# Kernel tuning notes

Measured on AMD Instinct MI355X. Metric: run time of the kernel, lower is better.

Reference implementation:

```python
import jax, jax.numpy as jnp
import numpy as np

B, N, G, E = 4, 8192, 512, 512
D = 3 * E  # fused channel dim = 1536
BN_EPS = 1e-5


def setup_inputs() -> dict:
    key = jax.random.key(0)
    ks = jax.random.split(key, 8)
    f32 = jnp.float32
    return {
        "xyz": jax.random.normal(ks[0], (B, N, 3), f32),
        "centers": jax.random.normal(ks[1], (B, G, 3), f32),
        "H4": jax.random.normal(ks[2], (B, G, E), f32),
        "H8": jax.random.normal(ks[3], (B, G, E), f32),
        "H12": jax.random.normal(ks[4], (B, G, E), f32),
        "w1": jax.random.normal(ks[5], (512, D), f32) * 0.02,
        "b1": jnp.zeros((512,), f32),
        "g1": jnp.ones((512,), f32),
        "be1": jnp.zeros((512,), f32),
        "m1": jnp.zeros((512,), f32),
        "v1": jnp.ones((512,), f32),
        "w2": jax.random.normal(ks[6], (512, 512), f32) * 0.02,
        "b2": jnp.zeros((512,), f32),
        "g2": jnp.ones((512,), f32),
        "be2": jnp.zeros((512,), f32),
        "m2": jnp.zeros((512,), f32),
        "v2": jnp.ones((512,), f32),
    }


def _bn(x, gamma, beta, mean, var):
    # BatchNorm1d, eval mode with running stats (per-channel, last axis)
    return (x - mean) * jax.lax.rsqrt(var + BN_EPS) * gamma + beta


def reference(xyz, centers, H4, H8, H12,
              w1, b1, g1, be1, m1, v1,
              w2, b2, g2, be2, m2, v2):
    fused = jnp.concatenate([H4, H8, H12], axis=-1)  # [B,G,D]
    # squared pairwise distances [B,N,G]
    d = (jnp.sum(xyz * xyz, axis=-1, keepdims=True)
         + jnp.sum(centers * centers, axis=-1)[:, None, :]
         - 2.0 * jnp.einsum('bnc,bgc->bng', xyz, centers))
    neg_d3, idx = jax.lax.top_k(-d, 3)  # 3 smallest distances, ascending
    d3 = -neg_d3  # [B,N,3]
    recip = 1.0 / (d3 + 1e-8)
    w = recip / jnp.sum(recip, axis=-1, keepdims=True)  # [B,N,3]
    # gather neighbor features: [B,N,3,D]
    gathered = jax.vmap(lambda f, i: f[i])(fused, idx)
    interp = jnp.einsum('bnk,bnkd->bnd', w, gathered)  # [B,N,D]
    # 1x1 conv == per-point linear; conv -> BN(eval) -> ReLU, twice
    h = jax.nn.relu(_bn(interp @ w1.T + b1, g1, be1, m1, v1))
    h = jax.nn.relu(_bn(h @ w2.T + b2, g2, be2, m2, v2))
    return h  # [B,N,512]
```

## Files before the change

kernel.cpp:

```cpp
#include <hip/hip_runtime.h>
#include <stdint.h>

#define NP 8192
#define NG 512
#define DF 1536

using f32x4    = __attribute__((ext_vector_type(4))) float;
using bf16x8   = __attribute__((ext_vector_type(8))) __bf16;
using ushort8v = __attribute__((ext_vector_type(8))) unsigned short;


__device__ __forceinline__ unsigned short f32_to_bf16(float f) {
  unsigned int u = __float_as_uint(f);
  u += 0x7fffu + ((u >> 16) & 1u);
  return (unsigned short)(u >> 16);
}
__device__ __forceinline__ float bf2f(unsigned short u) {
  return __uint_as_float(((unsigned)u) << 16);
}

struct FusedArgs {
  const float *xyz, *centers, *H4, *H8, *H12, *w1, *w2;
  const float *g1, *be1, *m1, *v1, *g2, *be2, *m2, *v2, *b1, *b2;
  unsigned short *fswz, *w1s, *w2s, *Amatb;
  int *nidx; float *nw, *s1, *t1, *s2, *t2;
  float *outp;
};

__device__ void phase_knn(const FusedArgs& a, char* smem, int w) {
  const int tid = threadIdx.x;
  float4* cs = (float4*)smem;
  const int b = w >> 7;
  for (int i = tid; i < NG; i += 256) {
    float c0 = a.centers[((size_t)b * NG + i) * 3 + 0];
    float c1 = a.centers[((size_t)b * NG + i) * 3 + 1];
    float c2 = a.centers[((size_t)b * NG + i) * 3 + 2];
    float4 v; v.x = c0; v.y = c1; v.z = c2; v.w = c0 * c0 + c1 * c1 + c2 * c2;
    cs[(i >> 7) * 129 + (i & 127)] = v;
  }
  __syncthreads();
  const int t = (w & 127) * 256 + tid;
  const int p = t >> 2, q = t & 3;
  const size_t pi = (size_t)b * NP + p;
  const float x0 = a.xyz[pi * 3 + 0], x1 = a.xyz[pi * 3 + 1], x2 = a.xyz[pi * 3 + 2];
  const float xx = x0 * x0 + x1 * x1 + x2 * x2;
  float d0 = 3.4e38f, d1 = 3.4e38f, d2 = 3.4e38f;
  int i0 = 0, i1 = 0, i2 = 0;
  const int gbase = q * 128;
  const float4* csq = cs + q * 129;
#pragma unroll 4
  for (int j = 0; j < 128; ++j) {
    float4 c = csq[j];
    float d = xx + c.w - 2.0f * (x0 * c.x + x1 * c.y + x2 * c.z);
    int g = gbase + j;
    bool c0 = d < d0, c1 = d < d1, c2 = d < d2;
    float nd2 = c1 ? d1 : (c2 ? d : d2); int ni2 = c1 ? i1 : (c2 ? g : i2);
    float nd1 = c0 ? d0 : (c1 ? d : d1); int ni1 = c0 ? i0 : (c1 ? g : i1);
    d0 = c0 ? d : d0;                    i0 = c0 ? g : i0;
    d1 = nd1; i1 = ni1; d2 = nd2; i2 = ni2;
  }
#pragma unroll
  for (int off = 1; off <= 2; off <<= 1) {
    float e0 = __shfl_xor(d0, off), e1 = __shfl_xor(d1, off), e2 = __shfl_xor(d2, off);
    int j0 = __shfl_xor(i0, off), j1 = __shfl_xor(i1, off), j2 = __shfl_xor(i2, off);
#pragma unroll
    for (int s = 0; s < 3; ++s) {
      float e = (s == 0) ? e0 : (s == 1 ? e1 : e2);
      int   j = (s == 0) ? j0 : (s == 1 ? j1 : j2);
      bool c0 = (e < d0) || (e == d0 && j < i0);
      bool c1 = (e < d1) || (e == d1 && j < i1);
      bool c2 = (e < d2) || (e == d2 && j < i2);
      float nd2 = c1 ? d1 : (c2 ? e : d2); int ni2 = c1 ? i1 : (c2 ? j : i2);
      float nd1 = c0 ? d0 : (c1 ? e : d1); int ni1 = c0 ? i0 : (c1 ? j : i1);
      d0 = c0 ? e : d0;                    i0 = c0 ? j : i0;
      d1 = nd1; i1 = ni1; d2 = nd2; i2 = ni2;
    }
  }
  if (q == 0) {
    float r0 = 1.0f / (d0 + 1e-8f), r1 = 1.0f / (d1 + 1e-8f), r2 = 1.0f / (d2 + 1e-8f);
    float inv = 1.0f / (r0 + r1 + r2);
    a.nw[pi * 3 + 0] = r0 * inv; a.nw[pi * 3 + 1] = r1 * inv; a.nw[pi * 3 + 2] = r2 * inv;
    a.nidx[pi * 3 + 0] = i0; a.nidx[pi * 3 + 1] = i1; a.nidx[pi * 3 + 2] = i2;
  }
}

__device__ void phase_casts(const FusedArgs& a, int u) {
  const int tid = threadIdx.x;
  if (u < 2048) {
    const int qd = (u - 512) * 256 + tid;
    const int L = qd & 63, t2 = qd >> 6;
    const int kc = t2 % 48, mg = t2 / 48;
    const int m = mg * 16 + (L & 15);
    const int k = kc * 32 + (L >> 4) * 8;
    const float* src = (k < 512) ? a.H4 : (k < 1024 ? a.H8 : a.H12);
    const float* sp = &src[(size_t)m * 512 + (k & 511)];
    float4 va = *(const float4*)sp, vb = *(const float4*)(sp + 4);
    ushort8v o;
    o[0] = f32_to_bf16(va.x); o[1] = f32_to_bf16(va.y);
    o[2] = f32_to_bf16(va.z); o[3] = f32_to_bf16(va.w);
    o[4] = f32_to_bf16(vb.x); o[5] = f32_to_bf16(vb.y);
    o[6] = f32_to_bf16(vb.z); o[7] = f32_to_bf16(vb.w);
    *(ushort8v*)&a.fswz[((size_t)(mg * 48 + kc)) * 512 + L * 8] = o;
  } else if (u < 2432) {
    const int qd = (u - 2048) * 256 + tid;
    const int L = qd & 63, t2 = qd >> 6;
    const int kc = t2 % 48, ng = t2 / 48;
    const int n = ng * 16 + (L & 15);
    const int k = kc * 32 + (L >> 4) * 8;
    const float* sp = &a.w1[(size_t)n * 1536 + k];
    float4 va = *(const float4*)sp, vb = *(const float4*)(sp + 4);
    ushort8v o;
    o[0] = f32_to_bf16(va.x); o[1] = f32_to_bf16(va.y);
    o[2] = f32_to_bf16(va.z); o[3] = f32_to_bf16(va.w);
    o[4] = f32_to_bf16(vb.x); o[5] = f32_to_bf16(vb.y);
    o[6] = f32_to_bf16(vb.z); o[7] = f32_to_bf16(vb.w);
    *(ushort8v*)&a.w1s[((size_t)(ng * 48 + kc)) * 512 + L * 8] = o;
  } else if (u < 2560) {
    const int qd = (u - 2432) * 256 + tid;
    const int L = qd & 63, t2 = qd >> 6;
    const int kc = t2 & 15, ng = t2 >> 4;
    const int n = ng * 16 + (L & 15);
    const int k = kc * 32 + (L >> 4) * 8;
    const float* sp = &a.w2[(size_t)n * 512 + k];
    float4 va = *(const float4*)sp, vb = *(const float4*)(sp + 4);
    ushort8v o;
    o[0] = f32_to_bf16(va.x); o[1] = f32_to_bf16(va.y);
    o[2] = f32_to_bf16(va.z); o[3] = f32_to_bf16(va.w);
    o[4] = f32_to_bf16(vb.x); o[5] = f32_to_bf16(vb.y);
    o[6] = f32_to_bf16(vb.z); o[7] = f32_to_bf16(vb.w);
    *(ushort8v*)&a.w2s[((size_t)(ng * 16 + kc)) * 512 + L * 8] = o;
  } else {
    for (int i = tid; i < 512; i += 256) {
      float sa = a.g1[i] / sqrtf(a.v1[i] + 1e-5f);
      a.s1[i] = sa; a.t1[i] = a.be1[i] - a.m1[i] * sa;
      float sb = a.g2[i] / sqrtf(a.v2[i] + 1e-5f);
      a.s2[i] = sb; a.t2[i] = a.be2[i] - a.m2[i] * sb;
    }
  }
}

__device__ void phase_gemm1(const FusedArgs& a, char* smem, int blk) {
  float* red = (float*)smem;
  const int tid = threadIdx.x, lane = tid & 63, wv = tid >> 6;
  const int m0 = (blk >> 3) * 32;
  const int n0 = (blk & 7) * 64;
  const unsigned short* Ap = a.fswz + ((size_t)(m0 >> 4) * 48 + wv * 12) * 512 + lane * 8;
  const unsigned short* Bp = a.w1s  + ((size_t)(n0 >> 4) * 48 + wv * 12) * 512 + lane * 8;

  f32x4 acc[2][4];
#pragma unroll
  for (int i = 0; i < 2; ++i)
#pragma unroll
    for (int j = 0; j < 4; ++j) acc[i][j] = (f32x4){0.f, 0.f, 0.f, 0.f};

  bf16x8 af[2], bfr[4], afn[2], bfn[4];
#pragma unroll
  for (int i = 0; i < 2; ++i)
    af[i]  = __builtin_bit_cast(bf16x8, *(const ushort8v*)(Ap + (size_t)i * 48 * 512));
#pragma unroll
  for (int i = 0; i < 4; ++i)
    bfr[i] = __builtin_bit_cast(bf16x8, *(const ushort8v*)(Bp + (size_t)i * 48 * 512));
#pragma unroll 1
  for (int kc = 0; kc < 12; ++kc) {
    if (kc < 11) {
#pragma unroll
      for (int i = 0; i < 2; ++i)
        afn[i] = __builtin_bit_cast(bf16x8, *(const ushort8v*)(Ap + (size_t)i * 48 * 512 + (kc + 1) * 512));
#pragma unroll
      for (int i = 0; i < 4; ++i)
        bfn[i] = __builtin_bit_cast(bf16x8, *(const ushort8v*)(Bp + (size_t)i * 48 * 512 + (kc + 1) * 512));
    }
#pragma unroll
    for (int mi = 0; mi < 2; ++mi)
#pragma unroll
      for (int ni = 0; ni < 4; ++ni)
        acc[mi][ni] = __builtin_amdgcn_mfma_f32_16x16x32_bf16(af[mi], bfr[ni], acc[mi][ni], 0, 0, 0);
#pragma unroll
    for (int i = 0; i < 2; ++i) af[i] = afn[i];
#pragma unroll
    for (int i = 0; i < 4; ++i) bfr[i] = bfn[i];
  }

  for (int w = 0; w < 4; ++w) {
    if (wv == w) {
#pragma unroll
      for (int mi = 0; mi < 2; ++mi)
#pragma unroll
        for (int ni = 0; ni < 4; ++ni) {
          int col = ni * 16 + (lane & 15);
#pragma unroll
          for (int r = 0; r < 4; ++r) {
            int row = mi * 16 + (lane >> 4) * 4 + r;
            if (w == 0) red[row * 65 + col] = acc[mi][ni][r];
            else        red[row * 65 + col] += acc[mi][ni][r];
          }
        }
    }
    __syncthreads();
  }
  const int row = tid >> 3;
  const int col = (tid & 7) * 8;
  ushort8v o;
#pragma unroll
  for (int j = 0; j < 8; ++j) {
    int n = n0 + col + j;
    float v = red[row * 65 + col + j];
    o[j] = f32_to_bf16(a.s1[n] * (v + a.b1[n]) + a.t1[n]);
  }
  *(ushort8v*)&a.Amatb[(size_t)(m0 + row) * 512 + n0 + col] = o;
}

__global__ __launch_bounds__(1024, 4) void k_mega(FusedArgs a) {
  __shared__ __align__(16) unsigned short hl[128 * 512];
  const int tid = threadIdx.x, lane = tid & 63, wv = tid >> 6;
  const int xcd = blockIdx.x & 7, slot = blockIdx.x >> 3;
  const int m0 = (xcd * 32 + slot) * 128;

  {
    const int rg = wv >> 1, kc0 = (wv & 1) * 8;
    const int p = m0 + rg * 16 + (lane & 15);
    const int b = p >> 13;
    const int i0 = a.nidx[p * 3 + 0], i1 = a.nidx[p * 3 + 1], i2 = a.nidx[p * 3 + 2];
    const float w0 = a.nw[p * 3 + 0], w1v = a.nw[p * 3 + 1], w2v = a.nw[p * 3 + 2];
    const int co = kc0 * 32 + (lane >> 4) * 8;
    const unsigned short* A0 = a.Amatb + ((size_t)(b * 512 + i0)) * 512 + co;
    const unsigned short* A1 = a.Amatb + ((size_t)(b * 512 + i1)) * 512 + co;
    const unsigned short* A2 = a.Amatb + ((size_t)(b * 512 + i2)) * 512 + co;
    unsigned short* wp = hl + (size_t)(rg * 16 + kc0) * 512 + lane * 8;
#pragma unroll 4
    for (int j = 0; j < 8; ++j) {
      ushort8v u0 = *(const ushort8v*)(A0 + j * 32);
      ushort8v u1 = *(const ushort8v*)(A1 + j * 32);
      ushort8v u2 = *(const ushort8v*)(A2 + j * 32);
      ushort8v o;
#pragma unroll
      for (int jj = 0; jj < 8; ++jj) {
        float v = w0 * bf2f(u0[jj]) + w1v * bf2f(u1[jj]) + w2v * bf2f(u2[jj]);
        o[jj] = f32_to_bf16(fmaxf(v, 0.f));
      }
      *(ushort8v*)(wp + (size_t)j * 512) = o;
    }
  }
  __syncthreads();

  const int n0 = wv * 32;
  const unsigned short* Bbase = a.w2s + (size_t)(n0 >> 4) * 16 * 512 + lane * 8;

  f32x4 acc[8][2];
#pragma unroll
  for (int i = 0; i < 8; ++i) {
    acc[i][0] = (f32x4){0.f, 0.f, 0.f, 0.f};
    acc[i][1] = (f32x4){0.f, 0.f, 0.f, 0.f};
  }

  bf16x8 bfr[2], bfn[2];
  bfr[0] = __builtin_bit_cast(bf16x8, *(const ushort8v*)(Bbase));
  bfr[1] = __builtin_bit_cast(bf16x8, *(const ushort8v*)(Bbase + (size_t)16 * 512));
#pragma unroll 1
  for (int kc = 0; kc < 16; ++kc) {
    if (kc < 15) {
      bfn[0] = __builtin_bit_cast(bf16x8,
          *(const ushort8v*)(Bbase + (size_t)(kc + 1) * 512));
      bfn[1] = __builtin_bit_cast(bf16x8,
          *(const ushort8v*)(Bbase + (size_t)(16 + kc + 1) * 512));
    }
#pragma unroll
    for (int mi = 0; mi < 8; ++mi) {
      bf16x8 af = __builtin_bit_cast(bf16x8,
          *(const ushort8v*)(hl + (size_t)(mi * 16 + kc) * 512 + lane * 8));
      acc[mi][0] = __builtin_amdgcn_mfma_f32_16x16x32_bf16(af, bfr[0], acc[mi][0], 0, 0, 0);
      acc[mi][1] = __builtin_amdgcn_mfma_f32_16x16x32_bf16(af, bfr[1], acc[mi][1], 0, 0, 0);
    }
    bfr[0] = bfn[0]; bfr[1] = bfn[1];
  }

#pragma unroll
  for (int mi = 0; mi < 8; ++mi) {
    int mbase = m0 + mi * 16 + (lane >> 4) * 4;
#pragma unroll
    for (int ni = 0; ni < 2; ++ni) {
      int n = n0 + ni * 16 + (lane & 15);
      float s = a.s2[n], bb = a.b2[n], t = a.t2[n];
      f32x4 v = acc[mi][ni];
#pragma unroll
      for (int r = 0; r < 4; ++r)
        __builtin_nontemporal_store(fmaxf(s * (v[r] + bb) + t, 0.f),
                                    &a.outp[(size_t)(mbase + r) * 512 + n]);
    }
  }
}

__global__ __launch_bounds__(256) void k_casts(FusedArgs a) {
  phase_casts(a, 512 + blockIdx.x);
}
__global__ __launch_bounds__(256) void k_g1knn(FusedArgs a) {
  __shared__ __align__(16) char smem[8448];
  if (blockIdx.x < 512) phase_gemm1(a, smem, blockIdx.x);
  else                  phase_knn(a, smem, blockIdx.x - 512);
}

extern "C" void kernel_launch(void* const* d_in, const int* in_sizes, int n_in,
                              void* d_out, int out_size, void* d_ws, size_t ws_size,
                              hipStream_t stream) {
  char* ws = (char*)d_ws;
  FusedArgs a;
  a.xyz     = (const float*)d_in[0];
  a.centers = (const float*)d_in[1];
  a.H4      = (const float*)d_in[2];
  a.H8      = (const float*)d_in[3];
  a.H12     = (const float*)d_in[4];
  a.w1      = (const float*)d_in[5];
  a.b1      = (const float*)d_in[6];
  a.g1      = (const float*)d_in[7];
  a.be1     = (const float*)d_in[8];
  a.m1      = (const float*)d_in[9];
  a.v1      = (const float*)d_in[10];
  a.w2      = (const float*)d_in[11];
  a.b2      = (const float*)d_in[12];
  a.g2      = (const float*)d_in[13];
  a.be2     = (const float*)d_in[14];
  a.m2      = (const float*)d_in[15];
  a.v2      = (const float*)d_in[16];
  a.fswz  = (unsigned short*)(ws);
  a.w1s   = (unsigned short*)(ws + 6291456);
  a.w2s   = (unsigned short*)(ws + 7864320);
  a.Amatb = (unsigned short*)(ws + 8388608);
  a.nidx  = (int*)           (ws + 10485760);
  a.nw    = (float*)         (ws + 10878976);
  a.s1    = (float*)         (ws + 11272192);
  a.t1 = a.s1 + 512; a.s2 = a.t1 + 512; a.t2 = a.s2 + 512;
  a.outp  = (float*)d_out;

  k_casts<<<2049, 256, 0, stream>>>(a);
  k_g1knn<<<1024, 256, 0, stream>>>(a);
  k_mega <<< 256, 1024, 0, stream>>>(a);
}
```

Baseline: 162.0 us.

## Pipeline neighbor gather into LDS with MFMA over K quarters

Splits the gather-interpolate-ReLU stage of the mega kernel into four K-quarters and interleaves them with the second GEMM. Each quarter's global loads are issued before the MFMA work on the previous quarter, so gather latency overlaps with matrix math instead of running as one serial phase. This adds three extra block-wide barriers and keeps more registers live for the in-flight loads, which may pressure occupancy at 1024 threads.

Result: slower. 179.0 us (+10.5%).

```diff
diff --git a/kernel.cpp b/kernel.cpp
--- a/kernel.cpp
+++ b/kernel.cpp
@@ -216,32 +216,16 @@
   const int xcd = blockIdx.x & 7, slot = blockIdx.x >> 3;
   const int m0 = (xcd * 32 + slot) * 128;
 
-  {
-    const int rg = wv >> 1, kc0 = (wv & 1) * 8;
-    const int p = m0 + rg * 16 + (lane & 15);
-    const int b = p >> 13;
-    const int i0 = a.nidx[p * 3 + 0], i1 = a.nidx[p * 3 + 1], i2 = a.nidx[p * 3 + 2];
-    const float w0 = a.nw[p * 3 + 0], w1v = a.nw[p * 3 + 1], w2v = a.nw[p * 3 + 2];
-    const int co = kc0 * 32 + (lane >> 4) * 8;
-    const unsigned short* A0 = a.Amatb + ((size_t)(b * 512 + i0)) * 512 + co;
-    const unsigned short* A1 = a.Amatb + ((size_t)(b * 512 + i1)) * 512 + co;
-    const unsigned short* A2 = a.Amatb + ((size_t)(b * 512 + i2)) * 512 + co;
-    unsigned short* wp = hl + (size_t)(rg * 16 + kc0) * 512 + lane * 8;
-#pragma unroll 4
-    for (int j = 0; j < 8; ++j) {
-      ushort8v u0 = *(const ushort8v*)(A0 + j * 32);
-      ushort8v u1 = *(const ushort8v*)(A1 + j * 32);
-      ushort8v u2 = *(const ushort8v*)(A2 + j * 32);
-      ushort8v o;
-#pragma unroll
-      for (int jj = 0; jj < 8; ++jj) {
-        float v = w0 * bf2f(u0[jj]) + w1v * bf2f(u1[jj]) + w2v * bf2f(u2[jj]);
-        o[jj] = f32_to_bf16(fmaxf(v, 0.f));
-      }
-      *(ushort8v*)(wp + (size_t)j * 512) = o;
-    }
-  }
-  __syncthreads();
+  const int rg = wv >> 1;
+  const int p = m0 + rg * 16 + (lane & 15);
+  const int b = p >> 13;
+  const int i0 = a.nidx[p * 3 + 0], i1 = a.nidx[p * 3 + 1], i2 = a.nidx[p * 3 + 2];
+  const float w0 = a.nw[p * 3 + 0], w1v = a.nw[p * 3 + 1], w2v = a.nw[p * 3 + 2];
+  const int cg8 = (lane >> 4) * 8;
+  const unsigned short* A0 = a.Amatb + ((size_t)(b * 512 + i0)) * 512 + cg8;
+  const unsigned short* A1 = a.Amatb + ((size_t)(b * 512 + i1)) * 512 + cg8;
+  const unsigned short* A2 = a.Amatb + ((size_t)(b * 512 + i2)) * 512 + cg8;
+  const int kcw = (wv & 1) * 2;
 
   const int n0 = wv * 32;
   const unsigned short* Bbase = a.w2s + (size_t)(n0 >> 4) * 16 * 512 + lane * 8;
@@ -253,26 +237,78 @@
     acc[i][1] = (f32x4){0.f, 0.f, 0.f, 0.f};
   }
 
-  bf16x8 bfr[2], bfn[2];
-  bfr[0] = __builtin_bit_cast(bf16x8, *(const ushort8v*)(Bbase));
-  bfr[1] = __builtin_bit_cast(bf16x8, *(const ushort8v*)(Bbase + (size_t)16 * 512));
-#pragma unroll 1
-  for (int kc = 0; kc < 16; ++kc) {
-    if (kc < 15) {
-      bfn[0] = __builtin_bit_cast(bf16x8,
-          *(const ushort8v*)(Bbase + (size_t)(kc + 1) * 512));
-      bfn[1] = __builtin_bit_cast(bf16x8,
-          *(const ushort8v*)(Bbase + (size_t)(16 + kc + 1) * 512));
-    }
-#pragma unroll
-    for (int mi = 0; mi < 8; ++mi) {
-      bf16x8 af = __builtin_bit_cast(bf16x8,
-          *(const ushort8v*)(hl + (size_t)(mi * 16 + kc) * 512 + lane * 8));
-      acc[mi][0] = __builtin_amdgcn_mfma_f32_16x16x32_bf16(af, bfr[0], acc[mi][0], 0, 0, 0);
-      acc[mi][1] = __builtin_amdgcn_mfma_f32_16x16x32_bf16(af, bfr[1], acc[mi][1], 0, 0, 0);
-    }
-    bfr[0] = bfn[0]; bfr[1] = bfn[1];
-  }
+  ushort8v u[2][3];
+  bf16x8 bcur[2], bnxt[2];
+
+#define ISSUE(q)                                                        \
+  {                                                                     \
+    _Pragma("unroll")                                                   \
+    for (int j = 0; j < 2; ++j) {                                       \
+      const int c = ((q) * 4 + kcw + j) * 32;                           \
+      u[j][0] = *(const ushort8v*)(A0 + c);                             \
+      u[j][1] = *(const ushort8v*)(A1 + c);                             \
+      u[j][2] = *(const ushort8v*)(A2 + c);                             \
+    }                                                                   \
+  }
+#define WRITE(q)                                                        \
+  {                                                                     \
+    _Pragma("unroll")                                                   \
+    for (int j = 0; j < 2; ++j) {                                       \
+      const int kc = (q) * 4 + kcw + j;                                 \
+      ushort8v o;                                                       \
+      _Pragma("unroll")                                                 \
+      for (int jj = 0; jj < 8; ++jj) {                                  \
+        float v = w0 * bf2f(u[j][0][jj]) + w1v * bf2f(u[j][1][jj])      \
+                + w2v * bf2f(u[j][2][jj]);                              \
+        o[jj] = f32_to_bf16(fmaxf(v, 0.f));                             \
+      }                                                                 \
+      *(ushort8v*)(hl + (size_t)(rg * 16 + kc) * 512 + lane * 8) = o;   \
+    }                                                                   \
+  }
+#define MFMAQ(q)                                                        \
+  {                                                                     \
+    _Pragma("unroll")                                                   \
+    for (int kk = 0; kk < 4; ++kk) {                                    \
+      const int kc = (q) * 4 + kk;                                      \
+      if (kc < 15) {                                                    \
+        bnxt[0] = __builtin_bit_cast(bf16x8,                            \
+            *(const ushort8v*)(Bbase + (size_t)(kc + 1) * 512));        \
+        bnxt[1] = __builtin_bit_cast(bf16x8,                            \
+            *(const ushort8v*)(Bbase + (size_t)(16 + kc + 1) * 512));   \
+      }                                                                 \
+      _Pragma("unroll")                                                 \
+      for (int mi = 0; mi < 8; ++mi) {                                  \
+        bf16x8 af = __builtin_bit_cast(bf16x8,                          \
+            *(const ushort8v*)(hl + (size_t)(mi * 16 + kc) * 512 + lane * 8)); \
+        acc[mi][0] = __builtin_amdgcn_mfma_f32_16x16x32_bf16(af, bcur[0], acc[mi][0], 0, 0, 0); \
+        acc[mi][1] = __builtin_amdgcn_mfma_f32_16x16x32_bf16(af, bcur[1], acc[mi][1], 0, 0, 0); \
+      }                                                                 \
+      if (kc < 15) { bcur[0] = bnxt[0]; bcur[1] = bnxt[1]; }            \
+    }                                                                   \
+  }
+
+  ISSUE(0);
+  bcur[0] = __builtin_bit_cast(bf16x8, *(const ushort8v*)(Bbase));
+  bcur[1] = __builtin_bit_cast(bf16x8, *(const ushort8v*)(Bbase + (size_t)16 * 512));
+  WRITE(0);
+  __syncthreads();
+  ISSUE(1);
+  MFMAQ(0);
+  WRITE(1);
+  __syncthreads();
+  ISSUE(2);
+  MFMAQ(1);
+  WRITE(2);
+  __syncthreads();
+  ISSUE(3);
+  MFMAQ(2);
+  WRITE(3);
+  __syncthreads();
+  MFMAQ(3);
+
+#undef ISSUE
+#undef WRITE
+#undef MFMAQ
 
 #pragma unroll
   for (int mi = 0; mi < 8; ++mi) {
```
